# Optimization experiments

Hardware: AMD Instinct MI355X
Metric: run time of the kernel (lower is better)

## Reference

```python
import jax, jax.numpy as jnp
import numpy as np
import math

D = 192            # base channel dim (init arg d); s has D channels
D2 = 2 * D         # y has 2d channels
H = 48; W = 48; BS = 2
NH = 8             # attention heads (divides both D2 and D)
NY = H * W         # tokens per image


def pe2d(d_model, height, width):
    """Faithful port of positionalencoding2d: (d_model, H, W)."""
    dh = d_model // 2
    div = jnp.exp(jnp.arange(0.0, dh, 2.0) * (-math.log(10000.0) / dh))  # (dh/2,)
    pw = jnp.arange(0.0, width)[:, None] * div    # (W, dh/2)
    ph = jnp.arange(0.0, height)[:, None] * div   # (H, dh/2)
    pe = jnp.zeros((d_model, height, width), jnp.float32)
    pe = pe.at[0:dh:2].set(jnp.broadcast_to(jnp.sin(pw).T[:, None, :], (dh // 2, height, width)))
    pe = pe.at[1:dh:2].set(jnp.broadcast_to(jnp.cos(pw).T[:, None, :], (dh // 2, height, width)))
    pe = pe.at[dh::2].set(jnp.broadcast_to(jnp.sin(ph).T[:, :, None], (dh // 2, height, width)))
    pe = pe.at[dh + 1::2].set(jnp.broadcast_to(jnp.cos(ph).T[:, :, None], (dh // 2, height, width)))
    return pe


def conv1x1(x, w, b):
    # x: (b,c,h,w), w: (out,c)
    return jnp.einsum('bchw,oc->bohw', x, w) + b[None, :, None, None]


def conv3x3(x, w, b):
    out = jax.lax.conv_general_dilated(x, w, (1, 1), 'SAME',
                                       dimension_numbers=('NCHW', 'OIHW', 'NCHW'))
    return out + b[None, :, None, None]


def bn(x, g, b):
    # inference-mode batchnorm with zero-mean / unit-var running stats
    return x * g[None, :, None, None] + b[None, :, None, None]


def setup_inputs() -> dict:
    key = jax.random.key(0)
    ks = jax.random.split(key, 8)
    r = lambda k, shp: jax.random.normal(k, shp, jnp.float32) * 0.02
    return {
        'y': jax.random.normal(ks[0], (BS, D2, H, W), jnp.float32),
        's': jax.random.normal(ks[1], (BS, D, H, W), jnp.float32),
        'wq_w': r(ks[2], (D2, D2)), 'wq_b': jnp.zeros((D2,), jnp.float32),
        'wk_w': r(ks[3], (D2, D2)), 'wk_b': jnp.zeros((D2,), jnp.float32),
        'wv_w': r(ks[4], (D, D)),   'wv_b': jnp.zeros((D,), jnp.float32),
        'conv1_w': r(ks[5], (D2, D2)), 'conv1_b': jnp.zeros((D2,), jnp.float32),
        'bn1_g': jnp.ones((D2,), jnp.float32), 'bn1_b': jnp.zeros((D2,), jnp.float32),
        'conv2_w': r(ks[6], (D, D)), 'conv2_b': jnp.zeros((D,), jnp.float32),
        'bn2_g': jnp.ones((D,), jnp.float32), 'bn2_b': jnp.zeros((D,), jnp.float32),
        'up_w': r(ks[7], (D2, D2, 3, 3)), 'up_b': jnp.zeros((D2,), jnp.float32),
        'conv3_w': r(jax.random.fold_in(key, 10), (D, D2)), 'conv3_b': jnp.zeros((D,), jnp.float32),
        'bn3_g': jnp.ones((D,), jnp.float32), 'bn3_b': jnp.zeros((D,), jnp.float32),
        'sig_w': r(jax.random.fold_in(key, 11), (D, D)), 'sig_b': jnp.zeros((D,), jnp.float32),
        'bnsig_g': jnp.ones((D,), jnp.float32), 'bnsig_b': jnp.zeros((D,), jnp.float32),
    }


def reference(y, s, wq_w, wq_b, wk_w, wk_b, wv_w, wv_b,
              conv1_w, conv1_b, bn1_g, bn1_b,
              conv2_w, conv2_b, bn2_g, bn2_b,
              up_w, up_b, conv3_w, conv3_b, bn3_g, bn3_b,
              sig_w, sig_b, bnsig_g, bnsig_b):
    bs = y.shape[0]
    y = y + pe2d(D2, H, W)[None]
    s = s + pe2d(D, H, W)[None]
    # conv+BN+ReLU feature extraction
    y_c1 = jax.nn.relu(bn(conv1x1(y, conv1_w, conv1_b), bn1_g, bn1_b))
    s_c2 = jax.nn.relu(bn(conv1x1(s, conv2_w, conv2_b), bn2_g, bn2_b))
    y_c3 = conv3x3(y, up_w, up_b)                                   # 'up' branch conv
    y_c3 = jax.nn.relu(bn(conv1x1(y_c3, conv3_w, conv3_b), bn3_g, bn3_b))  # (b, D, H, W)
    # tokenize
    yt = y_c1.reshape(bs, D2, NY).transpose(0, 2, 1)   # (b, ny, 2d)
    st = s_c2.reshape(bs, D, NY).transpose(0, 2, 1)    # (b, ny, d)
    # multi-head cross attention: Q,K from y-tokens, V from s-tokens
    Q = (yt @ wq_w.T + wq_b).reshape(bs, NY, NH, D2 // NH).transpose(0, 2, 1, 3)  # (b,h,ny,2d/h)
    K = (yt @ wk_w.T + wk_b).reshape(bs, NY, NH, D2 // NH).transpose(0, 2, 1, 3)
    V = (st @ wv_w.T + wv_b).reshape(bs, NY, NH, D // NH).transpose(0, 2, 1, 3)   # (b,h,ny,d/h)
    M = jnp.einsum('bhnd,bhmd->bhnm', Q, K) / math.sqrt(D)  # scale = d**0.5 as in source
    A = jax.nn.softmax(M, axis=-1)
    Z = jnp.einsum('bhnm,bhmd->bhnd', A, V)                 # (b,h,ny,d/h)
    Z = Z.transpose(0, 2, 1, 3).reshape(bs, NY, D).transpose(0, 2, 1).reshape(bs, D, H, W)
    # sigmoid gate and fuse
    g = jax.nn.sigmoid(bn(conv1x1(Z, sig_w, sig_b), bnsig_g, bnsig_b))
    Z = g * s
    return jnp.concatenate([Z, y_c3], axis=1)               # (b, 2d, H, W)
```

## Files before the change

### kernel.cpp

```cpp
#include <hip/hip_runtime.h>
#include <hip/hip_bf16.h>

#define Dc   192
#define D2c  384
#define NYc  2304

#define QSCALE 0.1041175462f

typedef __attribute__((ext_vector_type(8))) short short8;
typedef __attribute__((ext_vector_type(4))) float f32x4;

__device__ __forceinline__ unsigned short f2bf(float f) {
    unsigned int u = __float_as_uint(f);
    u += 0x7FFFu + ((u >> 16) & 1u);
    return (unsigned short)(u >> 16);
}
__device__ __forceinline__ float bf2f(unsigned short u) {
    return __uint_as_float((unsigned)u << 16);
}
__device__ __forceinline__ float fexp2(float x) {
    float r; asm("v_exp_f32 %0, %1" : "=v"(r) : "v"(x)); return r;
}
__device__ __forceinline__ unsigned cvtpk(float lo, float hi) {
    unsigned r; asm("v_cvt_pk_bf16_f32 %0, %1, %2" : "=v"(r) : "v"(lo), "v"(hi));
    return r;
}
__device__ __forceinline__ int swzb(int orig, int nwg) {
    int q = nwg >> 3, r = nwg & 7, x = orig & 7;
    int base = (x < r) ? x * (q + 1) : r * (q + 1) + (x - r) * q;
    return base + (orig >> 3);
}

__global__ __launch_bounds__(256)
void build_pe_kernel(float* __restrict__ peY, float* __restrict__ peS) {
    int idx = blockIdx.x * 256 + threadIdx.x;
    int c, p, C; float* dst; int off;
    if (idx < 18432) { c = idx / 48; p = idx % 48; C = 384; dst = peY; off = idx; }
    else { int k = idx - 18432; c = k / 48; p = k % 48; C = 192; dst = peS; off = k; }
    int dh = C >> 1;
    int i = ((c < dh) ? c : c - dh) >> 1;
    float divv = expf((float)(2 * i) * (-9.210340371976184f / (float)dh));
    float ang = (float)p * divv;
    dst[off] = (c & 1) ? cosf(ang) : sinf(ang);
}

__global__ __launch_bounds__(256)
void prep_pe_kernel(const float* __restrict__ y, const float* __restrict__ s,
                    const float* __restrict__ peY, const float* __restrict__ peS,
                    unsigned short* __restrict__ ytok, unsigned short* __restrict__ stok,
                    float* __restrict__ sch) {
    __shared__ unsigned short T[64][66];
    int bid = blockIdx.x;
    int b, ct, nt, C; const float* in; const float* pe; unsigned short* outp; bool isS;
    if (bid < 432) { isS = false; b = bid / 216; int r = bid % 216; ct = r / 36; nt = r % 36;
                     in = y; pe = peY; outp = ytok; C = 384; }
    else { int l = bid - 432; isS = true; b = l / 108; int r = l % 108; ct = r / 36; nt = r % 36;
           in = s; pe = peS; outp = stok; C = 192; }
    int t = threadIdx.x;
    int nl = t & 63;
    int n = nt * 64 + nl;
    int pos_x = n % 48, pos_y = n / 48;
    #pragma unroll
    for (int i = 0; i < 16; ++i) {
        int cl = (t >> 6) + 4 * i;
        int c = ct * 64 + cl;
        int pos = (c < (C >> 1)) ? pos_x : pos_y;
        long gi = (long)b * C * NYc + (long)c * NYc + n;
        float v = in[gi] + pe[c * 48 + pos];
        if (isS) sch[gi] = v;
        T[nl][cl] = f2bf(v);
    }
    __syncthreads();
    #pragma unroll
    for (int i = 0; i < 8; ++i) {
        int nl2 = (t >> 5) + 8 * i;
        int cp  = t & 31;
        unsigned u = (unsigned)T[nl2][2 * cp] | ((unsigned)T[nl2][2 * cp + 1] << 16);
        long row = (long)b * NYc + nt * 64 + nl2;
        *(unsigned*)(outp + row * C + ct * 64 + 2 * cp) = u;
    }
}

__global__ __launch_bounds__(256)
void prep_w_kernel(const float* __restrict__ w0, const float* __restrict__ w1,
                   const float* __restrict__ w2, const float* __restrict__ w3,
                   const float* __restrict__ w4, const float* __restrict__ w5,
                   const float* __restrict__ w6, unsigned short* __restrict__ dst,
                   const float* __restrict__ wq_b, const float* __restrict__ wk_b,
                   float* __restrict__ qkb,
                   const float* __restrict__ upw, unsigned short* __restrict__ upT,
                   const float* __restrict__ up_b, const float* __restrict__ conv3_b,
                   float* __restrict__ c3b) {
    int idx = blockIdx.x * 256 + threadIdx.x;
    if (idx < 626688) {
        if (idx < 768)
            qkb[idx] = (idx < 384) ? wq_b[idx] * QSCALE : wk_b[idx - 384];
        const float* src; int off; float scl = 1.0f;
        if      (idx < 147456) { src = w0; off = idx; }
        else if (idx < 294912) { src = w1; off = idx - 147456; scl = QSCALE; }
        else if (idx < 442368) { src = w2; off = idx - 294912; }
        else if (idx < 479232) { src = w3; off = idx - 442368; }
        else if (idx < 516096) { src = w4; off = idx - 479232; }
        else if (idx < 552960) { src = w5; off = idx - 516096; }
        else                   { src = w6; off = idx - 552960; }
        dst[idx] = f2bf(src[off] * scl);
    } else if (idx < 1953792) {
        int k = idx - 626688;
        int j = k / 384, m = k % 384;
        int tap = j / 384, c = j % 384;
        upT[k] = f2bf(upw[((long)m * 384 + c) * 9 + tap]);
    } else if (idx < 1953984) {
        int o = idx - 1953792;
        float acc = 0.f;
        for (int m = 0; m < 384; ++m) acc += w6[o * 384 + m] * up_b[m];
        c3b[o] = acc + conv3_b[o];
    }
}

struct Seg {
    const unsigned short* A; const unsigned short* B;
    int aP, bP, K, nT, blkOff, nBlk, flags, nSplit;
    long oSplitBytes;
    const float *bias, *bng, *bnb;
    char* out; int oPitch; long oBatch;
};

template<int NSEG>
__global__ __launch_bounds__(256)
void fused_gemm(Seg s0, Seg s1, Seg s2, const float* __restrict__ smul)
{
    int raw = blockIdx.x;
    Seg sg = s0;
    if (NSEG > 1 && raw >= s1.blkOff) sg = s1;
    if (NSEG > 2 && raw >= s2.blkOff) sg = s2;
    int local = swzb(raw - sg.blkOff, sg.nBlk);
    int kBase = 0;
    if (sg.nSplit > 1) {
        int pc = sg.nBlk / sg.nSplit;
        int g = local / pc; local -= g * pc;
        sg.A += (long)g * sg.K;
        sg.out += (long)g * sg.oSplitBytes;
        kBase = g * sg.K;
    }
    int mt = local / sg.nT, nt = local - mt * sg.nT;
    int m0 = mt * 64, n0 = nt * 64;

    __shared__ __align__(16) unsigned short As[2][64][72];
    __shared__ __align__(16) unsigned short Bs[2][64][72];

    int t = threadIdx.x, lane = t & 63, w = t >> 6;
    int lr = lane & 15, lg = lane >> 4;
    int wm = (w >> 1) * 32, wn = (w & 1) * 32;

    f32x4 acc[2][2];
    #pragma unroll
    for (int i = 0; i < 2; ++i)
        #pragma unroll
        for (int j = 0; j < 2; ++j)
            acc[i][j] = (f32x4){0.f, 0.f, 0.f, 0.f};

    uint4 ra[2], rb[2];
    bool im2colB = (sg.flags & 1) != 0;

    auto load = [&](int k0) {
        #pragma unroll
        for (int i = 0; i < 2; ++i) {
            int idx = t + i * 256, row = idx >> 3, sl = idx & 7;
            ra[i] = *(const uint4*)(sg.A + (long)(m0 + row) * sg.aP + k0 + sl * 8);
            if (im2colB) {
                int tok = n0 + row;
                int bb = tok >= NYc;
                int n = tok - bb * NYc;
                int kk = kBase + k0;
                int tap = kk / 384;
                int rem = kk - tap * 384 + sl * 8;
                int py = n / 48 + tap / 3 - 1;
                int px = n % 48 + tap % 3 - 1;
                rb[i] = (py >= 0 && py < 48 && px >= 0 && px < 48)
                    ? *(const uint4*)(sg.B + ((long)bb * NYc + py * 48 + px) * sg.bP + rem)
                    : make_uint4(0, 0, 0, 0);
            } else {
                rb[i] = *(const uint4*)(sg.B + (long)(n0 + row) * sg.bP + k0 + sl * 8);
            }
        }
    };
    auto store = [&](int buf) {
        #pragma unroll
        for (int i = 0; i < 2; ++i) {
            int idx = t + i * 256;
            *(uint4*)&As[buf][idx >> 3][(idx & 7) * 8] = ra[i];
            *(uint4*)&Bs[buf][idx >> 3][(idx & 7) * 8] = rb[i];
        }
    };

    load(0); store(0); __syncthreads();
    int NT = sg.K >> 6;
    int cur = 0;
    for (int tt = 0; tt < NT; ++tt) {
        bool more = (tt + 1 < NT);
        if (more) load((tt + 1) << 6);
        #pragma unroll
        for (int kk = 0; kk < 2; ++kk) {
            short8 a0 = *(const short8*)&As[cur][wm + lr][kk * 32 + lg * 8];
            short8 a1 = *(const short8*)&As[cur][wm + 16 + lr][kk * 32 + lg * 8];
            short8 b0 = *(const short8*)&Bs[cur][wn + lr][kk * 32 + lg * 8];
            short8 b1 = *(const short8*)&Bs[cur][wn + 16 + lr][kk * 32 + lg * 8];
            acc[0][0] = __builtin_amdgcn_mfma_f32_16x16x32_bf16(a0, b0, acc[0][0], 0, 0, 0);
            acc[0][1] = __builtin_amdgcn_mfma_f32_16x16x32_bf16(a0, b1, acc[0][1], 0, 0, 0);
            acc[1][0] = __builtin_amdgcn_mfma_f32_16x16x32_bf16(a1, b0, acc[1][0], 0, 0, 0);
            acc[1][1] = __builtin_amdgcn_mfma_f32_16x16x32_bf16(a1, b1, acc[1][1], 0, 0, 0);
        }
        if (more) store(cur ^ 1);
        __syncthreads();
        cur ^= 1;
    }

    #pragma unroll
    for (int i = 0; i < 2; ++i)
    #pragma unroll
    for (int j = 0; j < 2; ++j)
    #pragma unroll
    for (int r = 0; r < 4; ++r) {
        int gm = m0 + wm + i * 16 + lg * 4 + r;
        int gn = n0 + wn + j * 16 + lr;
        int ch = (sg.flags & 8) ? gm : gn;
        float v = acc[i][j][r];
        if (!(sg.flags & 32)) v += sg.bias[ch];
        if (sg.flags & 2)
            v = fmaxf(fmaf(v, sg.bng[ch], sg.bnb[ch]), 0.f);
        long o; int b = 0, tok = gn;
        if (sg.flags & 8) {
            b = gn >= NYc; tok = gn - b * NYc;
            o = (long)b * sg.oBatch + (long)gm * sg.oPitch + tok;
        } else {
            o = (long)gm * sg.oPitch + gn;
        }
        if (sg.flags & 16) {
            v = fmaf(v, sg.bng[ch], sg.bnb[ch]);
            v = 1.f / (1.f + __expf(-v));
            v *= smul[(long)b * 442368 + (long)gm * NYc + tok];
        }
        if (sg.flags & 4) ((float*)sg.out)[o] = v;
        else              ((unsigned short*)sg.out)[o] = f2bf(v);
    }
}

__global__ __launch_bounds__(256)
void reduce_up_kernel(const unsigned short* __restrict__ part,
                      const float* __restrict__ c3b,
                      const float* __restrict__ bn3g, const float* __restrict__ bn3b,
                      float* __restrict__ out) {
    int tid = blockIdx.x * 256 + threadIdx.x;
    int e = tid * 4;
    int b = e / 442368; int r = e - b * 442368;
    int o = r / 2304;
    ushort4 p0 = *(const ushort4*)(part + e);
    ushort4 p1 = *(const ushort4*)(part + 884736 + e);
    ushort4 p2 = *(const ushort4*)(part + 1769472 + e);
    float g = bn3g[o], bb = bn3b[o], cb = c3b[o];
    float4 res;
    float* rp = (float*)&res;
    unsigned short* q0 = (unsigned short*)&p0;
    unsigned short* q1 = (unsigned short*)&p1;
    unsigned short* q2 = (unsigned short*)&p2;
    #pragma unroll
    for (int j = 0; j < 4; ++j) {
        float v = bf2f(q0[j]) + bf2f(q1[j]) + bf2f(q2[j]) + cb;
        rp[j] = fmaxf(fmaf(v, g, bb), 0.f);
    }
    *(float4*)(out + (long)b * 884736 + 442368 + r) = res;
}

__global__ __launch_bounds__(512)
void attn_kernel(const unsigned short* __restrict__ QK,
                 const unsigned short* __restrict__ Vc,
                 unsigned short* __restrict__ Zt)
{
    int nid = swzb(blockIdx.x, 576);
    int qb = nid % 36;
    int bh = nid / 36;
    int b = bh >> 3, h = bh & 7;
    const unsigned short* Qg = QK + (long)b * NYc * 768 + h * 48;
    const unsigned short* Kg = Qg + 384;
    const unsigned short* Vg = Vc + ((long)b * Dc + h * 24) * NYc;
    unsigned short*       Z  = Zt + (long)b * NYc * Dc + h * 24;

    __shared__ __align__(16) unsigned short Ks_[128][72];
    __shared__ __align__(16) unsigned short Vs_[32][136];
    __shared__ __align__(16) unsigned int   Ps_[8][16][36];

    int t = threadIdx.x, lane = t & 63, w = t >> 6;
    int lr = lane & 15, lg = lane >> 4;
    int tm = w >> 1, hf = w & 1;
    int q0 = qb * 64;

    short8 z8 = {0, 0, 0, 0, 0, 0, 0, 0};
    const unsigned short* qrow = Qg + (long)(q0 + tm * 16 + lr) * 768;
    short8 bq0 = *(const short8*)(qrow + lg * 8);
    short8 bq1 = (lg < 2) ? *(const short8*)(qrow + 32 + lg * 8) : z8;

    float m_run = -1e30f, l_run = 0.f;
    f32x4 O0 = {0.f, 0.f, 0.f, 0.f}, O1 = {0.f, 0.f, 0.f, 0.f};

    for (int kt = 0; kt < 18; ++kt) {
        long k0 = kt * 128;
        #pragma unroll
        for (int i = 0; i < 2; ++i) {
            int idx = t + i * 512;
            int row = idx >> 3, sl = idx & 7;
            uint4 v = make_uint4(0, 0, 0, 0);
            if (sl < 6) v = *(const uint4*)(Kg + (k0 + row) * 768 + sl * 8);
            *(uint4*)&Ks_[row][sl * 8] = v;
        }
        if (t < 384) {
            int row = t >> 4, sl = t & 15;
            *(uint4*)&Vs_[row][sl * 8] =
                *(const uint4*)(Vg + (long)row * NYc + k0 + sl * 8);
        }
        __syncthreads();

        f32x4 sS[4];
        #pragma unroll
        for (int ks = 0; ks < 4; ++ks) {
            short8 ak0 = *(const short8*)&Ks_[hf * 64 + ks * 16 + lr][lg * 8];
            short8 ak1 = *(const short8*)&Ks_[hf * 64 + ks * 16 + lr][32 + lg * 8];
            f32x4 c = {0.f, 0.f, 0.f, 0.f};
            c = __builtin_amdgcn_mfma_f32_16x16x32_bf16(ak0, bq0, c, 0, 0, 0);
            c = __builtin_amdgcn_mfma_f32_16x16x32_bf16(ak1, bq1, c, 0, 0, 0);
            sS[ks] = c;
        }

        float tmax = -1e30f;
        #pragma unroll
        for (int ks = 0; ks < 4; ++ks)
            #pragma unroll
            for (int r = 0; r < 4; ++r) tmax = fmaxf(tmax, sS[ks][r]);
        tmax = fmaxf(tmax, __shfl_xor(tmax, 16));
        tmax = fmaxf(tmax, __shfl_xor(tmax, 32));

        if (__any(tmax > m_run + 10.f)) {
            float mn = fmaxf(m_run, tmax);
            float al = fexp2(m_run - mn);
            m_run = mn;
            l_run *= al;
            #pragma unroll
            for (int rr = 0; rr < 4; ++rr) {
                float arr = __shfl(al, (lane & 48) | (lg * 4 + rr));
                O0[rr] *= arr; O1[rr] *= arr;
            }
        }

        float psum = 0.f;
        #pragma unroll
        for (int ks = 0; ks < 4; ++ks) {
            float p0 = fexp2(sS[ks][0] - m_run);
            float p1 = fexp2(sS[ks][1] - m_run);
            float p2 = fexp2(sS[ks][2] - m_run);
            float p3 = fexp2(sS[ks][3] - m_run);
            psum += (p0 + p1) + (p2 + p3);
            Ps_[w][lr][8 * ks + 2 * lg]     = cvtpk(p0, p1);
            Ps_[w][lr][8 * ks + 2 * lg + 1] = cvtpk(p2, p3);
        }
        psum += __shfl_xor(psum, 16);
        psum += __shfl_xor(psum, 32);
        l_run += psum;

        short8 ap0 = *(const short8*)&Ps_[w][lr][4 * lg];
        short8 ap1 = *(const short8*)&Ps_[w][lr][16 + 4 * lg];
        short8 bv00 = *(const short8*)&Vs_[lr][hf * 64 + lg * 8];
        short8 bv01 = *(const short8*)&Vs_[lr][hf * 64 + 32 + lg * 8];
        short8 bv10 = *(const short8*)&Vs_[16 + lr][hf * 64 + lg * 8];
        short8 bv11 = *(const short8*)&Vs_[16 + lr][hf * 64 + 32 + lg * 8];
        O0 = __builtin_amdgcn_mfma_f32_16x16x32_bf16(ap0, bv00, O0, 0, 0, 0);
        O0 = __builtin_amdgcn_mfma_f32_16x16x32_bf16(ap1, bv01, O0, 0, 0, 0);
        O1 = __builtin_amdgcn_mfma_f32_16x16x32_bf16(ap0, bv10, O1, 0, 0, 0);
        O1 = __builtin_amdgcn_mfma_f32_16x16x32_bf16(ap1, bv11, O1, 0, 0, 0);
        __syncthreads();
    }

    float* Cf = (float*)&Ps_[0][0][0];
    float* T = Cf + tm * 576;
    if (hf == 1) {
        #pragma unroll
        for (int j = 0; j < 4; ++j) {
            T[lane * 8 + j]     = O0[j];
            T[lane * 8 + 4 + j] = O1[j];
        }
        if (lane < 16) { T[512 + lane] = m_run; T[528 + lane] = l_run; }
    }
    __syncthreads();
    if (hf == 0) {
        float mB = T[512 + lr], lB = T[528 + lr];
        float mS = fmaxf(m_run, mB);
        float aA = fexp2(m_run - mS), aB = fexp2(mB - mS);
        float invl = 1.f / (l_run * aA + lB * aB);
        float fA = aA * invl, fB = aB * invl;
        #pragma unroll
        for (int rr = 0; rr < 4; ++rr) {
            int src = (lane & 48) | (lg * 4 + rr);
            float gA = __shfl(fA, src), gB = __shfl(fB, src);
            int n = q0 + tm * 16 + lg * 4 + rr;
            unsigned short* zr = Z + (long)n * Dc;
            float z0 = O0[rr] * gA + T[lane * 8 + rr] * gB;
            zr[lr] = f2bf(z0);
            if (lr < 8) {
                float z1 = O1[rr] * gA + T[lane * 8 + 4 + rr] * gB;
                zr[16 + lr] = f2bf(z1);
            }
        }
    }
}

extern "C" void kernel_launch(void* const* d_in, const int* in_sizes, int n_in,
                              void* d_out, int out_size, void* d_ws, size_t ws_size,
                              hipStream_t stream) {
    const float* y       = (const float*)d_in[0];
    const float* s       = (const float*)d_in[1];
    const float* wq_w    = (const float*)d_in[2];
    const float* wq_b    = (const float*)d_in[3];
    const float* wk_w    = (const float*)d_in[4];
    const float* wk_b    = (const float*)d_in[5];
    const float* wv_w    = (const float*)d_in[6];
    const float* wv_b    = (const float*)d_in[7];
    const float* conv1_w = (const float*)d_in[8];
    const float* conv1_b = (const float*)d_in[9];
    const float* bn1_g   = (const float*)d_in[10];
    const float* bn1_b   = (const float*)d_in[11];
    const float* conv2_w = (const float*)d_in[12];
    const float* conv2_b = (const float*)d_in[13];
    const float* bn2_g   = (const float*)d_in[14];
    const float* bn2_b   = (const float*)d_in[15];
    const float* up_w    = (const float*)d_in[16];
    const float* up_b    = (const float*)d_in[17];
    const float* conv3_w = (const float*)d_in[18];
    const float* conv3_b = (const float*)d_in[19];
    const float* bn3_g   = (const float*)d_in[20];
    const float* bn3_b   = (const float*)d_in[21];
    const float* sig_w   = (const float*)d_in[22];
    const float* sig_b   = (const float*)d_in[23];
    const float* bnsig_g = (const float*)d_in[24];
    const float* bnsig_b = (const float*)d_in[25];

    unsigned short* wsp   = (unsigned short*)d_ws;
    unsigned short* wcvt  = wsp;
    unsigned short* upT   = wcvt + 626688;
    unsigned short* Wc    = upT + 1327104;
    unsigned short* y_pe  = Wc + 663552;
    unsigned short* s_pe  = y_pe + 1769472;
    unsigned short* y_c1  = s_pe + 884736;
    unsigned short* s_c2  = y_c1 + 1769472;
    unsigned short* QKtok = s_c2 + 884736;
    unsigned short* Vch   = QKtok + 3538944;
    unsigned short* partZ = Vch + 884736;
    unsigned short* Ztok  = partZ;
    float*          s_ch  = (float*)(partZ + 2654208);
    float*          qkb   = s_ch + 884736;
    float*          c3b   = qkb + 768;
    float*          peY   = c3b + 192;
    float*          peS   = peY + 18432;

    const unsigned short* conv1wb = wcvt;
    const unsigned short* wqkb    = wcvt + 147456;
    const unsigned short* conv2wb = wcvt + 442368;
    const unsigned short* wvb     = wcvt + 479232;
    const unsigned short* sigwb   = wcvt + 516096;
    const unsigned short* conv3wb = wcvt + 552960;

    build_pe_kernel<<<108, 256, 0, stream>>>(peY, peS);
    prep_w_kernel<<<7633, 256, 0, stream>>>(conv1_w, wq_w, wk_w, conv2_w,
                                            wv_w, sig_w, conv3_w, wcvt,
                                            wq_b, wk_b, qkb, up_w, upT,
                                            up_b, conv3_b, c3b);
    prep_pe_kernel<<<648, 256, 0, stream>>>(y, s, peY, peS, y_pe, s_pe, s_ch);

    Seg sz = {};

    {
        Seg a = { conv3wb, upT, 384, 384, 384, 54, 0, 162, 32, 1, 0,
                  nullptr, nullptr, nullptr, (char*)Wc, 3456, 0 };
        fused_gemm<1><<<162, 256, 0, stream>>>(a, sz, sz, nullptr);
    }
    {
        Seg a = { Wc, y_pe, 3456, 384, 1152, 72, 0, 648, 1 | 8 | 32, 3,
                  (long)884736 * 2,
                  nullptr, nullptr, nullptr, (char*)partZ, NYc, 442368 };
        Seg b = { y_pe, conv1wb, 384, 384, 384, 6, 648, 432, 2, 1, 0,
                  conv1_b, bn1_g, bn1_b, (char*)y_c1, 384, 0 };
        Seg c = { s_pe, conv2wb, 192, 192, 192, 3, 1080, 216, 2, 1, 0,
                  conv2_b, bn2_g, bn2_b, (char*)s_c2, 192, 0 };
        fused_gemm<3><<<1296, 256, 0, stream>>>(a, b, c, nullptr);
    }
    {
        Seg a = { y_c1, wqkb, 384, 384, 384, 12, 0, 864, 0, 1, 0,
                  qkb, nullptr, nullptr, (char*)QKtok, 768, 0 };
        Seg b = { wvb, s_c2, 192, 192, 192, 72, 864, 216, 8, 1, 0,
                  wv_b, nullptr, nullptr, (char*)Vch, NYc, 442368 };
        fused_gemm<2><<<1080, 256, 0, stream>>>(a, b, sz, nullptr);
    }
    reduce_up_kernel<<<864, 256, 0, stream>>>(partZ, c3b, bn3_g, bn3_b,
                                              (float*)d_out);
    attn_kernel<<<576, 512, 0, stream>>>(QKtok, Vch, Ztok);
    {
        Seg a = { sigwb, Ztok, 192, 192, 192, 72, 0, 216, 4 | 8 | 16, 1, 0,
                  sig_b, bnsig_g, bnsig_b, (char*)d_out, NYc, 884736 };
        fused_gemm<1><<<216, 256, 0, stream>>>(a, sz, sz, s_ch);
    }
}
```

Measured before the change: 187.0 us.

## Load attention K/V tiles straight from global into MFMA registers, dropping LDS staging

The attention kernel no longer stages K and V tiles in shared memory. Each wave now reads its K rows and V columns from global memory directly into MFMA operand registers, which removes both per-iteration __syncthreads barriers; only the small per-wave P buffer stays in LDS. Blocks shrink to 256 threads covering 32 queries, so twice as many blocks launch and use much less LDS each, which should help occupancy. The cost is more redundant global/L2 traffic, since each K/V tile is now fetched by more waves and blocks, and the strided 16-byte row loads are poorly coalesced.

```diff
diff --git a/kernel.cpp b/kernel.cpp
--- a/kernel.cpp
+++ b/kernel.cpp
@@ -271,28 +271,26 @@
     *(float4*)(out + (long)b * 884736 + 442368 + r) = res;
 }
 
-__global__ __launch_bounds__(512)
+__global__ __launch_bounds__(256)
 void attn_kernel(const unsigned short* __restrict__ QK,
                  const unsigned short* __restrict__ Vc,
                  unsigned short* __restrict__ Zt)
 {
-    int nid = swzb(blockIdx.x, 576);
-    int qb = nid % 36;
-    int bh = nid / 36;
+    int nid = swzb(blockIdx.x, 1152);
+    int qb = nid % 72;
+    int bh = nid / 72;
     int b = bh >> 3, h = bh & 7;
     const unsigned short* Qg = QK + (long)b * NYc * 768 + h * 48;
     const unsigned short* Kg = Qg + 384;
     const unsigned short* Vg = Vc + ((long)b * Dc + h * 24) * NYc;
     unsigned short*       Z  = Zt + (long)b * NYc * Dc + h * 24;
 
-    __shared__ __align__(16) unsigned short Ks_[128][72];
-    __shared__ __align__(16) unsigned short Vs_[32][136];
-    __shared__ __align__(16) unsigned int   Ps_[8][16][36];
+    __shared__ __align__(16) uint2 Ps8[4][16][18];
 
     int t = threadIdx.x, lane = t & 63, w = t >> 6;
     int lr = lane & 15, lg = lane >> 4;
     int tm = w >> 1, hf = w & 1;
-    int q0 = qb * 64;
+    int q0 = qb * 32;
 
     short8 z8 = {0, 0, 0, 0, 0, 0, 0, 0};
     const unsigned short* qrow = Qg + (long)(q0 + tm * 16 + lr) * 768;
@@ -303,31 +301,28 @@
     f32x4 O0 = {0.f, 0.f, 0.f, 0.f}, O1 = {0.f, 0.f, 0.f, 0.f};
 
     for (int kt = 0; kt < 18; ++kt) {
-        long k0 = kt * 128;
-        #pragma unroll
-        for (int i = 0; i < 2; ++i) {
-            int idx = t + i * 512;
-            int row = idx >> 3, sl = idx & 7;
-            uint4 v = make_uint4(0, 0, 0, 0);
-            if (sl < 6) v = *(const uint4*)(Kg + (k0 + row) * 768 + sl * 8);
-            *(uint4*)&Ks_[row][sl * 8] = v;
-        }
-        if (t < 384) {
-            int row = t >> 4, sl = t & 15;
-            *(uint4*)&Vs_[row][sl * 8] =
-                *(const uint4*)(Vg + (long)row * NYc + k0 + sl * 8);
-        }
-        __syncthreads();
+        long k0 = (long)kt * 128 + hf * 64;
 
         f32x4 sS[4];
         #pragma unroll
         for (int ks = 0; ks < 4; ++ks) {
-            short8 ak0 = *(const short8*)&Ks_[hf * 64 + ks * 16 + lr][lg * 8];
-            short8 ak1 = *(const short8*)&Ks_[hf * 64 + ks * 16 + lr][32 + lg * 8];
+            const unsigned short* krow = Kg + (k0 + ks * 16 + lr) * 768 + lg * 8;
+            short8 ak0 = *(const short8*)krow;
+            short8 ak1 = (lg < 2) ? *(const short8*)(krow + 32) : z8;
             f32x4 c = {0.f, 0.f, 0.f, 0.f};
             c = __builtin_amdgcn_mfma_f32_16x16x32_bf16(ak0, bq0, c, 0, 0, 0);
             c = __builtin_amdgcn_mfma_f32_16x16x32_bf16(ak1, bq1, c, 0, 0, 0);
             sS[ks] = c;
+        }
+
+        const unsigned short* vrow0 = Vg + (long)lr * NYc + k0 + lg * 8;
+        short8 bv00 = *(const short8*)vrow0;
+        short8 bv01 = *(const short8*)(vrow0 + 32);
+        short8 bv10 = z8, bv11 = z8;
+        if (lr < 8) {
+            const unsigned short* vrow1 = vrow0 + (long)16 * NYc;
+            bv10 = *(const short8*)vrow1;
+            bv11 = *(const short8*)(vrow1 + 32);
         }
 
         float tmax = -1e30f;
@@ -358,27 +353,24 @@
             float p2 = fexp2(sS[ks][2] - m_run);
             float p3 = fexp2(sS[ks][3] - m_run);
             psum += (p0 + p1) + (p2 + p3);
-            Ps_[w][lr][8 * ks + 2 * lg]     = cvtpk(p0, p1);
-            Ps_[w][lr][8 * ks + 2 * lg + 1] = cvtpk(p2, p3);
+            uint2 u = { cvtpk(p0, p1), cvtpk(p2, p3) };
+            Ps8[w][lr][4 * ks + lg] = u;
         }
         psum += __shfl_xor(psum, 16);
         psum += __shfl_xor(psum, 32);
         l_run += psum;
 
-        short8 ap0 = *(const short8*)&Ps_[w][lr][4 * lg];
-        short8 ap1 = *(const short8*)&Ps_[w][lr][16 + 4 * lg];
-        short8 bv00 = *(const short8*)&Vs_[lr][hf * 64 + lg * 8];
-        short8 bv01 = *(const short8*)&Vs_[lr][hf * 64 + 32 + lg * 8];
-        short8 bv10 = *(const short8*)&Vs_[16 + lr][hf * 64 + lg * 8];
-        short8 bv11 = *(const short8*)&Vs_[16 + lr][hf * 64 + 32 + lg * 8];
+        short8 ap0 = *(const short8*)&Ps8[w][lr][2 * lg];
+        short8 ap1 = *(const short8*)&Ps8[w][lr][8 + 2 * lg];
         O0 = __builtin_amdgcn_mfma_f32_16x16x32_bf16(ap0, bv00, O0, 0, 0, 0);
         O0 = __builtin_amdgcn_mfma_f32_16x16x32_bf16(ap1, bv01, O0, 0, 0, 0);
         O1 = __builtin_amdgcn_mfma_f32_16x16x32_bf16(ap0, bv10, O1, 0, 0, 0);
         O1 = __builtin_amdgcn_mfma_f32_16x16x32_bf16(ap1, bv11, O1, 0, 0, 0);
-        __syncthreads();
-    }
-
-    float* Cf = (float*)&Ps_[0][0][0];
+    }
+
+    __syncthreads();
+
+    float* Cf = (float*)&Ps8[0][0][0];
     float* T = Cf + tm * 576;
     if (hf == 1) {
         #pragma unroll
@@ -499,7 +491,7 @@
     }
     reduce_up_kernel<<<864, 256, 0, stream>>>(partZ, c3b, bn3_g, bn3_b,
                                               (float*)d_out);
-    attn_kernel<<<576, 512, 0, stream>>>(QKtok, Vch, Ztok);
+    attn_kernel<<<1152, 256, 0, stream>>>(QKtok, Vch, Ztok);
     {
         Seg a = { sigwb, Ztok, 192, 192, 192, 72, 0, 216, 4 | 8 | 16, 1, 0,
                   sig_b, bnsig_g, bnsig_b, (char*)d_out, NYc, 884736 };
```

Measured after the change: 239.1 us. 1.28x slower.
